# Performance work log

Measured on AMD Instinct MI355X. Metric: run time of the kernel, lower is better.

Reference implementation:

```python
import jax, jax.numpy as jnp
import numpy as np

EMBED = 768
HEADS = 12
FFN = 3072
EPS = 1e-5

def _linear_params(key, din, dout):
    k1, k2 = jax.random.split(key)
    s = 1.0 / np.sqrt(din)
    W = jax.random.uniform(k1, (din, dout), minval=-s, maxval=s, dtype=jnp.float32)
    b = jax.random.uniform(k2, (dout,), minval=-s, maxval=s, dtype=jnp.float32)
    return W, b

def setup_inputs() -> dict:
    key = jax.random.key(0)
    ks = jax.random.split(key, 8)
    x = jax.random.normal(ks[0], (1, 4096, EMBED), dtype=jnp.float32)
    Wq, bq = _linear_params(ks[1], EMBED, EMBED)
    Wk, bk = _linear_params(ks[2], EMBED, EMBED)
    Wv, bv = _linear_params(ks[3], EMBED, EMBED)
    Wo, bo = _linear_params(ks[4], EMBED, EMBED)
    W1, b1 = _linear_params(ks[5], EMBED, FFN)
    W2, b2 = _linear_params(ks[6], FFN, EMBED)
    ln1_g = jnp.ones((EMBED,), jnp.float32); ln1_b = jnp.zeros((EMBED,), jnp.float32)
    ln2_g = jnp.ones((EMBED,), jnp.float32); ln2_b = jnp.zeros((EMBED,), jnp.float32)
    return {"x": x, "Wq": Wq, "bq": bq, "Wk": Wk, "bk": bk, "Wv": Wv, "bv": bv,
            "Wo": Wo, "bo": bo, "ln1_g": ln1_g, "ln1_b": ln1_b,
            "ln2_g": ln2_g, "ln2_b": ln2_b, "W1": W1, "b1": b1, "W2": W2, "b2": b2}

def _layernorm(x, g, b):
    mu = jnp.mean(x, axis=-1, keepdims=True)
    var = jnp.mean(jnp.square(x - mu), axis=-1, keepdims=True)
    return (x - mu) * jax.lax.rsqrt(var + EPS) * g + b

def _block(x, Wq, bq, Wk, bk, Wv, bv, Wo, bo, ln1_g, ln1_b, ln2_g, ln2_b, W1, b1, W2, b2):
    B, T, C = x.shape
    H = HEADS
    D = C // H
    # pre-LN
    h = _layernorm(x, ln1_g, ln1_b)
    # naive causal self-attention with explicit [B,H,T,T] scores (as in source)
    q = (h @ Wq + bq).reshape(B, T, H, D).transpose(0, 2, 1, 3)  # bhtd
    k = (h @ Wk + bk).reshape(B, T, H, D).transpose(0, 2, 1, 3)
    v = (h @ Wv + bv).reshape(B, T, H, D).transpose(0, 2, 1, 3)
    scores = jnp.einsum('bhqd,bhkd->bhqk', q, k) / jnp.sqrt(jnp.float32(D))
    causal = jnp.tril(jnp.ones((T, T), dtype=bool))  # True = keep
    scores = jnp.where(causal, scores, -jnp.inf)
    attn = jax.nn.softmax(scores, axis=-1)
    ctx = jnp.einsum('bhqk,bhkd->bhqd', attn, v)
    ctx = ctx.transpose(0, 2, 1, 3).reshape(B, T, C)
    y = ctx @ Wo + bo
    x = y + h  # residual onto ln1 output (source adds to post-LN x)
    # second LN + MLP
    h2 = _layernorm(x, ln2_g, ln2_b)
    m = jax.nn.gelu(h2 @ W1 + b1, approximate=False) @ W2 + b2
    return m + h2

def reference(x, Wq, bq, Wk, bk, Wv, bv, Wo, bo, ln1_g, ln1_b, ln2_g, ln2_b, W1, b1, W2, b2):
    return _block(x, Wq, bq, Wk, bk, Wv, bv, Wo, bo, ln1_g, ln1_b, ln2_g, ln2_b, W1, b1, W2, b2)
```

## Files before the change

kernel.cpp:

```cpp
#include <hip/hip_runtime.h>
#include <math.h>

#define EMBED 768
#define FFN_D 3072
#define TSEQ 4096
#define NHEAD 12
#define DHEAD 64
#define CQKV 2304
#define NSPLIT 4
#define NQITEMS 192
#define SC2Q 0.180336880111120419f

typedef _Float16 f16;
typedef __attribute__((ext_vector_type(2))) _Float16 f16x2;
typedef __attribute__((ext_vector_type(4))) _Float16 f16x4;
typedef __attribute__((ext_vector_type(8))) _Float16 f16x8;
typedef __attribute__((ext_vector_type(4))) float f32x4;

#if __has_builtin(__builtin_amdgcn_exp2f)
#define EXP2(x) __builtin_amdgcn_exp2f(x)
#else
#define EXP2(x) exp2f(x)
#endif

__device__ __forceinline__ f16x2 pkrtz(float a, float b) {
    return __builtin_bit_cast(f16x2, __builtin_amdgcn_cvt_pkrtz(a, b));
}

__device__ __forceinline__ void gload16(const f16* g, f16* lds) {
    __builtin_amdgcn_global_load_lds((const __attribute__((address_space(1))) void*)g,
                                     (__attribute__((address_space(3))) void*)lds, 16, 0, 0);
}

__global__ __launch_bounds__(256) void prep_kernel(const float* __restrict__ Wq,
                                                   const float* __restrict__ Wk,
                                                   const float* __restrict__ Wv,
                                                   const float* __restrict__ Wo,
                                                   const float* __restrict__ W1,
                                                   const float* __restrict__ W2,
                                                   const float* __restrict__ bq,
                                                   const float* __restrict__ bk,
                                                   const float* __restrict__ bv,
                                                   f16* __restrict__ WqkvT,
                                                   f16* __restrict__ WoT,
                                                   f16* __restrict__ W1T,
                                                   f16* __restrict__ W2T,
                                                   float* __restrict__ bqkv) {
    const int b = blockIdx.x;
    const int t = threadIdx.x;
    if (b == 1728) {
#pragma unroll
        for (int i = 0; i < 9; i++) {
            int idx = i * 256 + t;
            if (idx < 768) bqkv[idx] = bq[idx];
            else if (idx < 1536) bqkv[idx] = bk[idx - 768];
            else if (idx < 2304) bqkv[idx] = bv[idx - 1536];
        }
        return;
    }
    const float* W; f16* WT; int din, dout, local;
    if (b < 144)       { W = Wq; WT = WqkvT;                 din = 768;  dout = 768;  local = b; }
    else if (b < 288)  { W = Wk; WT = WqkvT + 768 * 768;     din = 768;  dout = 768;  local = b - 144; }
    else if (b < 432)  { W = Wv; WT = WqkvT + 2 * 768 * 768; din = 768;  dout = 768;  local = b - 288; }
    else if (b < 576)  { W = Wo; WT = WoT;                   din = 768;  dout = 768;  local = b - 432; }
    else if (b < 1152) { W = W1; WT = W1T;                   din = 768;  dout = 3072; local = b - 576; }
    else               { W = W2; WT = W2T;                   din = 3072; dout = 768;  local = b - 1152; }
    const int ntx = dout / 64;
    const int j0 = (local % ntx) * 64;
    const int i0 = (local / ntx) * 64;
    __shared__ float tile[64][65];
    const int tx = t & 63;
    const int ty = t >> 6;
#pragma unroll
    for (int rr = ty; rr < 64; rr += 4)
        tile[rr][tx] = W[(size_t)(i0 + rr) * dout + j0 + tx];
    __syncthreads();
    const int half = t & 31;
    const int rw = t >> 5;
#pragma unroll
    for (int rr = rw; rr < 64; rr += 8) {
        f16x2 v = {(f16)tile[2 * half][rr], (f16)tile[2 * half + 1][rr]};
        *(f16x2*)&WT[(size_t)(j0 + rr) * din + i0 + 2 * half] = v;
    }
}

__global__ __launch_bounds__(256) void ln_kernel(const float* __restrict__ x,
                                                 const float* __restrict__ g,
                                                 const float* __restrict__ b,
                                                 f16* __restrict__ hh) {
    const int row = blockIdx.x;
    const float* xr = x + (size_t)row * EMBED;
    const int t = threadIdx.x;
    float v0 = xr[t], v1 = xr[t + 256], v2 = xr[t + 512];
    float s = v0 + v1 + v2;
#pragma unroll
    for (int m = 1; m < 64; m <<= 1) s += __shfl_xor(s, m);
    __shared__ float red[4], red2[4];
    const int wid = t >> 6, lane = t & 63;
    if (lane == 0) red[wid] = s;
    __syncthreads();
    float mean = (red[0] + red[1] + red[2] + red[3]) * (1.0f / 768.0f);
    float d0 = v0 - mean, d1 = v1 - mean, d2 = v2 - mean;
    float ss = d0 * d0 + d1 * d1 + d2 * d2;
#pragma unroll
    for (int m = 1; m < 64; m <<= 1) ss += __shfl_xor(ss, m);
    if (lane == 0) red2[wid] = ss;
    __syncthreads();
    float inv = rsqrtf((red2[0] + red2[1] + red2[2] + red2[3]) * (1.0f / 768.0f) + 1e-5f);
    size_t base = (size_t)row * EMBED;
    hh[base + t]       = (f16)(d0 * inv * g[t] + b[t]);
    hh[base + t + 256] = (f16)(d1 * inv * g[t + 256] + b[t + 256]);
    hh[base + t + 512] = (f16)(d2 * inv * g[t + 512] + b[t + 512]);
}

template <int EPI, int BM, int BN>
__global__ __launch_bounds__(256) void gemm_kernel(const f16* __restrict__ A,
                                                   const f16* __restrict__ BT,
                                                   const float* __restrict__ bias,
                                                   const f16* __restrict__ resh,
                                                   float* __restrict__ outf,
                                                   f16* __restrict__ outh,
                                                   f16* __restrict__ vtout,
                                                   int M, int N, int K) {
    constexpr int IM = BM / 32;
    constexpr int JN = BN / 32;
    __shared__ __align__(16) f16 As[BM][64];
    __shared__ __align__(16) f16 Bs[BN][64];
    const int t = threadIdx.x;
    const int m0 = blockIdx.y * BM;
    const int n0 = blockIdx.x * BN;
    const int wid = t >> 6;
    const int lane = t & 63;
    const int wm = (wid >> 1) * (BM / 2);
    const int wn = (wid & 1) * (BN / 2);
    const int lr = lane & 15;
    const int quad = lane >> 4;
    const int sr = lane >> 3;
    const int scn = (lane & 7) ^ sr;
    const int xv = lr & 7;

    f32x4 zero = {0.f, 0.f, 0.f, 0.f};
    f32x4 acc[IM][JN];
#pragma unroll
    for (int i = 0; i < IM; i++)
#pragma unroll
        for (int j = 0; j < JN; j++) acc[i][j] = zero;

    const f16* Ap = A + (size_t)(m0 + wid * (BM / 4) + sr) * K + scn * 8;
    const f16* Bp = BT + (size_t)(n0 + wid * (BN / 4) + sr) * K + scn * 8;

    for (int k0 = 0; k0 < K; k0 += 64) {
        __syncthreads();
#pragma unroll
        for (int c = 0; c < BM / 32; c++)
            gload16(Ap + (size_t)(c * 8) * K + k0, &As[wid * (BM / 4) + c * 8][0]);
#pragma unroll
        for (int c = 0; c < BN / 32; c++)
            gload16(Bp + (size_t)(c * 8) * K + k0, &Bs[wid * (BN / 4) + c * 8][0]);
        __syncthreads();
#pragma unroll
        for (int ks = 0; ks < 2; ks++) {
            f16x8 af[IM], bf[JN];
#pragma unroll
            for (int i = 0; i < IM; i++)
                af[i] = *(const f16x8*)&As[wm + i * 16 + lr][((ks * 4 + quad) ^ xv) * 8];
#pragma unroll
            for (int j = 0; j < JN; j++)
                bf[j] = *(const f16x8*)&Bs[wn + j * 16 + lr][((ks * 4 + quad) ^ xv) * 8];
#pragma unroll
            for (int i = 0; i < IM; i++)
#pragma unroll
                for (int j = 0; j < JN; j++)
                    acc[i][j] = __builtin_amdgcn_mfma_f32_16x16x32_f16(bf[j], af[i], acc[i][j], 0, 0, 0);
        }
    }

    const bool vsec = (EPI == 0) && (n0 >= 2 * EMBED);
#pragma unroll
    for (int i = 0; i < IM; i++) {
        const int row = m0 + wm + i * 16 + lr;
#pragma unroll
        for (int j = 0; j < JN; j++) {
            const int col = n0 + wn + j * 16 + quad * 4;
            const float4 bv = *(const float4*)&bias[col];
            float v0 = acc[i][j][0] + bv.x;
            float v1 = acc[i][j][1] + bv.y;
            float v2 = acc[i][j][2] + bv.z;
            float v3 = acc[i][j][3] + bv.w;
            const size_t idx = (size_t)row * N + col;
            if (EPI == 0) {
                if (vsec) {
                    const int c0 = col - 2 * EMBED;
                    vtout[(size_t)(c0 + 0) * TSEQ + row] = (f16)v0;
                    vtout[(size_t)(c0 + 1) * TSEQ + row] = (f16)v1;
                    vtout[(size_t)(c0 + 2) * TSEQ + row] = (f16)v2;
                    vtout[(size_t)(c0 + 3) * TSEQ + row] = (f16)v3;
                } else {
                    const float qs = (col < EMBED) ? SC2Q : 1.0f;
                    f16x4 hv = {(f16)(v0 * qs), (f16)(v1 * qs), (f16)(v2 * qs), (f16)(v3 * qs)};
                    *(f16x4*)&outh[idx] = hv;
                }
            } else if (EPI == 1) {
                const f16x4 rr = *(const f16x4*)&resh[idx];
                f32x4 ov = {v0 + (float)rr[0], v1 + (float)rr[1], v2 + (float)rr[2], v3 + (float)rr[3]};
                *(f32x4*)&outf[idx] = ov;
            } else {
                f16x4 hv = {(f16)(0.5f * v0 * (1.0f + erff(v0 * 0.70710678118654752f))),
                            (f16)(0.5f * v1 * (1.0f + erff(v1 * 0.70710678118654752f))),
                            (f16)(0.5f * v2 * (1.0f + erff(v2 * 0.70710678118654752f))),
                            (f16)(0.5f * v3 * (1.0f + erff(v3 * 0.70710678118654752f)))};
                *(f16x4*)&outh[idx] = hv;
            }
        }
    }
}

__global__ __launch_bounds__(256) void attn_kernel(const f16* __restrict__ qkv,
                                                   const f16* __restrict__ vT,
                                                   f16* __restrict__ OpartH,
                                                   float2* __restrict__ ml,
                                                   int* __restrict__ ctr) {
    __shared__ __align__(16) f16 Ks[2][64][72];
    __shared__ __align__(16) f16 Vt[2][64][72];
    __shared__ int s_item;
    const int t = threadIdx.x;
    const int wid = t >> 6;
    const int lane = t & 63;
    const int lr = lane & 15;
    const int quad = lane >> 4;
    const int srow = t >> 3;
    const int scol = (t & 7) * 8;
    const int pA = (t & 1) * 16 + ((t >> 1) & 1) * 4 + (t & 4) * 8;
    const int xq = blockIdx.x & 7;

    for (;;) {
        __syncthreads();
        if (t == 0) s_item = atomicAdd(&ctr[xq], 1);
        __syncthreads();
        const int item = s_item;
        if (item >= NQITEMS) return;
        const int qb = 31 - item / 6;
        const int u = xq * 6 + item % 6;
        const int h = u >> 2;
        const int sp = u & 3;
        const int q0 = qb * 128;

        const int nkb = 2 * qb + 2;
        const int chunk = (nkb + NSPLIT - 1) / NSPLIT;
        const int kb0 = sp * chunk;
        const int kb1 = min(nkb, kb0 + chunk);
        const int wrow0 = q0 + wid * 32;

        float m_i[2] = {-INFINITY, -INFINITY};
        float l_lane[2] = {0.f, 0.f};
        f32x4 zero = {0.f, 0.f, 0.f, 0.f};
        f32x4 o[4][2];
#pragma unroll
        for (int dt = 0; dt < 4; dt++)
#pragma unroll
            for (int qt = 0; qt < 2; qt++) o[dt][qt] = zero;

        f16x8 qf[2][2];
        int4 kreg[2], vreg[2];
        const f16* kbase = qkv + EMBED + (size_t)h * DHEAD;
        const f16* vbase = vT + (size_t)h * DHEAD * TSEQ;
        if (kb0 < kb1) {
#pragma unroll
            for (int qt = 0; qt < 2; qt++)
#pragma unroll
                for (int dh = 0; dh < 2; dh++)
                    qf[qt][dh] = *(const f16x8*)(qkv + (size_t)(wrow0 + qt * 16 + lr) * CQKV
                                                 + h * DHEAD + dh * 32 + quad * 8);
            const int k0 = kb0 * 64;
#pragma unroll
            for (int p = 0; p < 2; p++) {
                kreg[p] = *(const int4*)(kbase + (size_t)(k0 + p * 32 + srow) * CQKV + scol);
                vreg[p] = *(const int4*)(vbase + (size_t)(p * 32 + srow) * TSEQ + k0 + scol);
            }
#pragma unroll
            for (int p = 0; p < 2; p++) {
                *(int4*)&Ks[0][p * 32 + srow][scol] = kreg[p];
                *(int2*)&Vt[0][p * 32 + srow][pA]     = make_int2(vreg[p].x, vreg[p].y);
                *(int2*)&Vt[0][p * 32 + srow][pA + 8] = make_int2(vreg[p].z, vreg[p].w);
            }
            if (kb0 + 1 < kb1) {
                const int kn = k0 + 64;
#pragma unroll
                for (int p = 0; p < 2; p++) {
                    kreg[p] = *(const int4*)(kbase + (size_t)(kn + p * 32 + srow) * CQKV + scol);
                    vreg[p] = *(const int4*)(vbase + (size_t)(p * 32 + srow) * TSEQ + kn + scol);
                }
            }
        }
        __syncthreads();

        int bsel = 0;
        for (int kb = kb0; kb < kb1; ++kb, bsel ^= 1) {
            const int k0 = kb * 64;
            if (kb + 1 < kb1) {
#pragma unroll
                for (int p = 0; p < 2; p++) {
                    *(int4*)&Ks[bsel ^ 1][p * 32 + srow][scol] = kreg[p];
                    *(int2*)&Vt[bsel ^ 1][p * 32 + srow][pA]     = make_int2(vreg[p].x, vreg[p].y);
                    *(int2*)&Vt[bsel ^ 1][p * 32 + srow][pA + 8] = make_int2(vreg[p].z, vreg[p].w);
                }
                if (kb + 2 < kb1) {
                    const int kn = (kb + 2) * 64;
#pragma unroll
                    for (int p = 0; p < 2; p++) {
                        kreg[p] = *(const int4*)(kbase + (size_t)(kn + p * 32 + srow) * CQKV + scol);
                        vreg[p] = *(const int4*)(vbase + (size_t)(p * 32 + srow) * TSEQ + kn + scol);
                    }
                }
            }

            if (k0 <= wrow0 + 31) {
                f32x4 s[4][2];
#pragma unroll
                for (int kt = 0; kt < 4; kt++)
#pragma unroll
                    for (int qt = 0; qt < 2; qt++) s[kt][qt] = zero;
                __builtin_amdgcn_s_setprio(1);
#pragma unroll
                for (int dh = 0; dh < 2; dh++) {
#pragma unroll
                    for (int kt = 0; kt < 4; kt++) {
                        f16x8 kf = *(const f16x8*)&Ks[bsel][kt * 16 + lr][dh * 32 + quad * 8];
#pragma unroll
                        for (int qt = 0; qt < 2; qt++)
                            s[kt][qt] = __builtin_amdgcn_mfma_f32_16x16x32_f16(kf, qf[qt][dh], s[kt][qt], 0, 0, 0);
                    }
                }
                __builtin_amdgcn_s_setprio(0);
                if (k0 + 63 > wrow0) {
#pragma unroll
                    for (int kt = 0; kt < 4; kt++)
#pragma unroll
                        for (int qt = 0; qt < 2; qt++)
#pragma unroll
                            for (int r = 0; r < 4; r++) {
                                int key = k0 + kt * 16 + quad * 4 + r;
                                int row = wrow0 + qt * 16 + lr;
                                if (key > row) s[kt][qt][r] = -INFINITY;
                            }
                }
                float mx[2];
#pragma unroll
                for (int qt = 0; qt < 2; qt++) {
                    float m = -INFINITY;
#pragma unroll
                    for (int kt = 0; kt < 4; kt++)
#pragma unroll
                        for (int r = 0; r < 4; r++) m = fmaxf(m, s[kt][qt][r]);
                    m = fmaxf(m, __shfl_xor(m, 16));
                    m = fmaxf(m, __shfl_xor(m, 32));
                    mx[qt] = m;
                }
                if (__any((mx[0] > m_i[0] + 4.f) || (mx[1] > m_i[1] + 4.f))) {
#pragma unroll
                    for (int qt = 0; qt < 2; qt++) {
                        float mn = fmaxf(m_i[qt], mx[qt]);
                        float al = EXP2(m_i[qt] - mn);
                        m_i[qt] = mn;
                        l_lane[qt] *= al;
#pragma unroll
                        for (int dt = 0; dt < 4; dt++)
#pragma unroll
                            for (int r = 0; r < 4; r++) o[dt][qt][r] *= al;
                    }
                }
                union PW { f16x8 v8; f16x2 h2[4]; };
                PW pw[2][2];
                float rs[2] = {0.f, 0.f};
#pragma unroll
                for (int kt = 0; kt < 4; kt++)
#pragma unroll
                    for (int qt = 0; qt < 2; qt++) {
                        float p0 = EXP2(s[kt][qt][0] - m_i[qt]);
                        float p1 = EXP2(s[kt][qt][1] - m_i[qt]);
                        float p2 = EXP2(s[kt][qt][2] - m_i[qt]);
                        float p3 = EXP2(s[kt][qt][3] - m_i[qt]);
                        rs[qt] += (p0 + p1) + (p2 + p3);
                        pw[kt >> 1][qt].h2[(kt & 1) * 2]     = pkrtz(p0, p1);
                        pw[kt >> 1][qt].h2[(kt & 1) * 2 + 1] = pkrtz(p2, p3);
                    }
#pragma unroll
                for (int qt = 0; qt < 2; qt++) l_lane[qt] += rs[qt];
                __builtin_amdgcn_s_setprio(1);
#pragma unroll
                for (int s2 = 0; s2 < 2; s2++)
#pragma unroll
                    for (int dt = 0; dt < 4; dt++) {
                        f16x8 vf = *(const f16x8*)&Vt[bsel][dt * 16 + lr][s2 * 32 + quad * 8];
#pragma unroll
                        for (int qt = 0; qt < 2; qt++)
                            o[dt][qt] = __builtin_amdgcn_mfma_f32_16x16x32_f16(vf, pw[s2][qt].v8, o[dt][qt], 0, 0, 0);
                    }
                __builtin_amdgcn_s_setprio(0);
            }
            __syncthreads();
        }

        float l_i[2];
#pragma unroll
        for (int qt = 0; qt < 2; qt++) {
            float v2 = l_lane[qt];
            v2 += __shfl_xor(v2, 16);
            v2 += __shfl_xor(v2, 32);
            l_i[qt] = v2;
        }
        f16* ob = &Ks[0][0][0] + wid * (32 * 72);
#pragma unroll
        for (int qt = 0; qt < 2; qt++)
#pragma unroll
            for (int dt = 0; dt < 4; dt++) {
                f16x4 oh = {(f16)o[dt][qt][0], (f16)o[dt][qt][1], (f16)o[dt][qt][2], (f16)o[dt][qt][3]};
                *(f16x4*)&ob[(qt * 16 + lr) * 72 + dt * 16 + quad * 4] = oh;
            }
        const int rl = lane >> 3;
        const int ck = lane & 7;
#pragma unroll
        for (int i = 0; i < 4; i++) {
            const int row_l = rl + i * 8;
            f16x8 val = *(const f16x8*)&ob[row_l * 72 + ck * 8];
            *(f16x8*)&OpartH[((size_t)sp * TSEQ + wrow0 + row_l) * EMBED + h * DHEAD + ck * 8] = val;
        }
#pragma unroll
        for (int qt = 0; qt < 2; qt++)
            if (quad == 0) {
                int row = wrow0 + qt * 16 + lr;
                ml[((size_t)sp * TSEQ + row) * NHEAD + h] = make_float2(m_i[qt], l_i[qt]);
            }
    }
}

__global__ __launch_bounds__(128) void attn_merge_kernel(const f16* __restrict__ OpartH,
                                                         const float2* __restrict__ ml,
                                                         f16* __restrict__ ctx) {
    const int row = blockIdx.x;
    const int t = threadIdx.x;
    __shared__ float wgt[NSPLIT][NHEAD];
    if (t < NHEAD) {
        float m[NSPLIT], l[NSPLIT];
        float M = -INFINITY;
#pragma unroll
        for (int s = 0; s < NSPLIT; s++) {
            float2 v = ml[((size_t)s * TSEQ + row) * NHEAD + t];
            m[s] = v.x; l[s] = v.y;
            M = fmaxf(M, m[s]);
        }
        float L = 0.f;
        float w[NSPLIT];
#pragma unroll
        for (int s = 0; s < NSPLIT; s++) {
            w[s] = exp2f(m[s] - M);
            L += l[s] * w[s];
        }
        float rL = 1.0f / L;
#pragma unroll
        for (int s = 0; s < NSPLIT; s++) wgt[s][t] = w[s] * rL;
    }
    __syncthreads();
    if (t < 96) {
        const int h = t >> 3;
        float acc[8] = {0.f, 0.f, 0.f, 0.f, 0.f, 0.f, 0.f, 0.f};
#pragma unroll
        for (int s = 0; s < NSPLIT; s++) {
            const float w = wgt[s][h];
            f16x8 v = *(const f16x8*)&OpartH[((size_t)s * TSEQ + row) * EMBED + t * 8];
#pragma unroll
            for (int e = 0; e < 8; e++) acc[e] += w * (float)v[e];
        }
        f16x8 out;
#pragma unroll
        for (int e = 0; e < 8; e++) out[e] = (f16)acc[e];
        *(f16x8*)&ctx[(size_t)row * EMBED + t * 8] = out;
    }
}

extern "C" void kernel_launch(void* const* d_in, const int* in_sizes, int n_in,
                              void* d_out, int out_size, void* d_ws, size_t ws_size,
                              hipStream_t stream) {
    const float* x     = (const float*)d_in[0];
    const float* Wq    = (const float*)d_in[1];
    const float* bq    = (const float*)d_in[2];
    const float* Wk    = (const float*)d_in[3];
    const float* bk    = (const float*)d_in[4];
    const float* Wv    = (const float*)d_in[5];
    const float* bv    = (const float*)d_in[6];
    const float* Wo    = (const float*)d_in[7];
    const float* bo    = (const float*)d_in[8];
    const float* ln1_g = (const float*)d_in[9];
    const float* ln1_b = (const float*)d_in[10];
    const float* ln2_g = (const float*)d_in[11];
    const float* ln2_b = (const float*)d_in[12];
    const float* W1    = (const float*)d_in[13];
    const float* b1    = (const float*)d_in[14];
    const float* W2    = (const float*)d_in[15];
    const float* b2    = (const float*)d_in[16];

    char* p = (char*)d_ws;
    auto alloc = [&](size_t bytes) -> void* {
        void* r = (void*)p;
        p += (bytes + 255) & ~(size_t)255;
        return r;
    };
    f16*   WqkvT = (f16*)alloc((size_t)CQKV * EMBED * 2);
    f16*   WoT   = (f16*)alloc((size_t)EMBED * EMBED * 2);
    f16*   W1T   = (f16*)alloc((size_t)FFN_D * EMBED * 2);
    f16*   W2T   = (f16*)alloc((size_t)EMBED * FFN_D * 2);
    float* bqkv  = (float*)alloc((size_t)CQKV * 4);
    f16*   hh    = (f16*)alloc((size_t)TSEQ * EMBED * 2);
    f16*   qkv   = (f16*)alloc((size_t)TSEQ * CQKV * 2);
    f16*   vT    = (f16*)alloc((size_t)EMBED * TSEQ * 2);
    f16*   ctx   = (f16*)alloc((size_t)TSEQ * EMBED * 2);
    float* x2    = (float*)alloc((size_t)TSEQ * EMBED * 4);
    f16*   h2h   = (f16*)alloc((size_t)TSEQ * EMBED * 2);
    f16*   m1    = (f16*)alloc((size_t)TSEQ * FFN_D * 2);
    int*   ctr   = (int*)alloc(256);

    f16*    OpartH = m1;
    float2* mlbuf  = (float2*)x2;

    dim3 blk(256);
    prep_kernel<<<dim3(1729), blk, 0, stream>>>(Wq, Wk, Wv, Wo, W1, W2, bq, bk, bv,
                                                WqkvT, WoT, W1T, W2T, bqkv);
    ln_kernel<<<dim3(TSEQ), blk, 0, stream>>>(x, ln1_g, ln1_b, hh);
    gemm_kernel<0, 128, 128><<<dim3(CQKV / 128, TSEQ / 128), blk, 0, stream>>>(
        hh, WqkvT, bqkv, nullptr, nullptr, qkv, vT, TSEQ, CQKV, EMBED);
    (void)hipMemsetAsync(ctr, 0, 256, stream);
    attn_kernel<<<dim3(1024), blk, 0, stream>>>(qkv, vT, OpartH, mlbuf, ctr);
    attn_merge_kernel<<<dim3(TSEQ), dim3(128), 0, stream>>>(OpartH, mlbuf, ctx);
    gemm_kernel<1, 128, 128><<<dim3(EMBED / 128, TSEQ / 128), blk, 0, stream>>>(
        ctx, WoT, bo, hh, x2, nullptr, nullptr, TSEQ, EMBED, EMBED);
    ln_kernel<<<dim3(TSEQ), blk, 0, stream>>>(x2, ln2_g, ln2_b, h2h);
    gemm_kernel<2, 128, 128><<<dim3(FFN_D / 128, TSEQ / 128), blk, 0, stream>>>(
        h2h, W1T, b1, nullptr, nullptr, m1, nullptr, TSEQ, FFN_D, EMBED);
    gemm_kernel<1, 128, 128><<<dim3(EMBED / 128, TSEQ / 128), blk, 0, stream>>>(
        m1, W2T, b2, h2h, (float*)d_out, nullptr, nullptr, TSEQ, EMBED, FFN_D);
}
```

Baseline: 353.2 us.

## Split attention KV range eightfold, single-buffer LDS for occupancy, narrow output GEMM tiles

```diff
diff --git a/kernel.cpp b/kernel.cpp
--- a/kernel.cpp
+++ b/kernel.cpp
@@ -7,8 +7,8 @@
 #define NHEAD 12
 #define DHEAD 64
 #define CQKV 2304
-#define NSPLIT 4
-#define NQITEMS 192
+#define NSPLIT 8
+#define NQITEMS 384
 #define SC2Q 0.180336880111120419f
 
 typedef _Float16 f16;
@@ -215,13 +215,13 @@
     }
 }
 
-__global__ __launch_bounds__(256) void attn_kernel(const f16* __restrict__ qkv,
-                                                   const f16* __restrict__ vT,
-                                                   f16* __restrict__ OpartH,
-                                                   float2* __restrict__ ml,
-                                                   int* __restrict__ ctr) {
-    __shared__ __align__(16) f16 Ks[2][64][72];
-    __shared__ __align__(16) f16 Vt[2][64][72];
+__global__ __launch_bounds__(256, 6) void attn_kernel(const f16* __restrict__ qkv,
+                                                      const f16* __restrict__ vT,
+                                                      f16* __restrict__ OpartH,
+                                                      float2* __restrict__ ml,
+                                                      int* __restrict__ ctr) {
+    __shared__ __align__(16) f16 Ks[64][72];
+    __shared__ __align__(16) f16 Vt[64][72];
     __shared__ int s_item;
     const int t = threadIdx.x;
     const int wid = t >> 6;
@@ -239,10 +239,10 @@
         __syncthreads();
         const int item = s_item;
         if (item >= NQITEMS) return;
-        const int qb = 31 - item / 6;
-        const int u = xq * 6 + item % 6;
-        const int h = u >> 2;
-        const int sp = u & 3;
+        const int qb = 31 - item / 12;
+        const int u = xq * 12 + item % 12;
+        const int h = u >> 3;
+        const int sp = u & 7;
         const int q0 = qb * 128;
 
         const int nkb = 2 * qb + 2;
@@ -277,42 +277,26 @@
                 kreg[p] = *(const int4*)(kbase + (size_t)(k0 + p * 32 + srow) * CQKV + scol);
                 vreg[p] = *(const int4*)(vbase + (size_t)(p * 32 + srow) * TSEQ + k0 + scol);
             }
+        }
+
+        for (int kb = kb0; kb < kb1; ++kb) {
+            const int k0 = kb * 64;
+            __syncthreads();
 #pragma unroll
             for (int p = 0; p < 2; p++) {
-                *(int4*)&Ks[0][p * 32 + srow][scol] = kreg[p];
-                *(int2*)&Vt[0][p * 32 + srow][pA]     = make_int2(vreg[p].x, vreg[p].y);
-                *(int2*)&Vt[0][p * 32 + srow][pA + 8] = make_int2(vreg[p].z, vreg[p].w);
-            }
-            if (kb0 + 1 < kb1) {
-                const int kn = k0 + 64;
+                *(int4*)&Ks[p * 32 + srow][scol] = kreg[p];
+                *(int2*)&Vt[p * 32 + srow][pA]     = make_int2(vreg[p].x, vreg[p].y);
+                *(int2*)&Vt[p * 32 + srow][pA + 8] = make_int2(vreg[p].z, vreg[p].w);
+            }
+            __syncthreads();
+            if (kb + 1 < kb1) {
+                const int kn = (kb + 1) * 64;
 #pragma unroll
                 for (int p = 0; p < 2; p++) {
                     kreg[p] = *(const int4*)(kbase + (size_t)(kn + p * 32 + srow) * CQKV + scol);
                     vreg[p] = *(const int4*)(vbase + (size_t)(p * 32 + srow) * TSEQ + kn + scol);
                 }
             }
-        }
-        __syncthreads();
-
-        int bsel = 0;
-        for (int kb = kb0; kb < kb1; ++kb, bsel ^= 1) {
-            const int k0 = kb * 64;
-            if (kb + 1 < kb1) {
-#pragma unroll
-                for (int p = 0; p < 2; p++) {
-                    *(int4*)&Ks[bsel ^ 1][p * 32 + srow][scol] = kreg[p];
-                    *(int2*)&Vt[bsel ^ 1][p * 32 + srow][pA]     = make_int2(vreg[p].x, vreg[p].y);
-                    *(int2*)&Vt[bsel ^ 1][p * 32 + srow][pA + 8] = make_int2(vreg[p].z, vreg[p].w);
-                }
-                if (kb + 2 < kb1) {
-                    const int kn = (kb + 2) * 64;
-#pragma unroll
-                    for (int p = 0; p < 2; p++) {
-                        kreg[p] = *(const int4*)(kbase + (size_t)(kn + p * 32 + srow) * CQKV + scol);
-                        vreg[p] = *(const int4*)(vbase + (size_t)(p * 32 + srow) * TSEQ + kn + scol);
-                    }
-                }
-            }
 
             if (k0 <= wrow0 + 31) {
                 f32x4 s[4][2];
@@ -320,18 +304,16 @@
                 for (int kt = 0; kt < 4; kt++)
 #pragma unroll
                     for (int qt = 0; qt < 2; qt++) s[kt][qt] = zero;
-                __builtin_amdgcn_s_setprio(1);
 #pragma unroll
                 for (int dh = 0; dh < 2; dh++) {
 #pragma unroll
                     for (int kt = 0; kt < 4; kt++) {
-                        f16x8 kf = *(const f16x8*)&Ks[bsel][kt * 16 + lr][dh * 32 + quad * 8];
+                        f16x8 kf = *(const f16x8*)&Ks[kt * 16 + lr][dh * 32 + quad * 8];
 #pragma unroll
                         for (int qt = 0; qt < 2; qt++)
                             s[kt][qt] = __builtin_amdgcn_mfma_f32_16x16x32_f16(kf, qf[qt][dh], s[kt][qt], 0, 0, 0);
                     }
                 }
-                __builtin_amdgcn_s_setprio(0);
                 if (k0 + 63 > wrow0) {
 #pragma unroll
                     for (int kt = 0; kt < 4; kt++)
@@ -386,19 +368,16 @@
                     }
 #pragma unroll
                 for (int qt = 0; qt < 2; qt++) l_lane[qt] += rs[qt];
-                __builtin_amdgcn_s_setprio(1);
 #pragma unroll
                 for (int s2 = 0; s2 < 2; s2++)
 #pragma unroll
                     for (int dt = 0; dt < 4; dt++) {
-                        f16x8 vf = *(const f16x8*)&Vt[bsel][dt * 16 + lr][s2 * 32 + quad * 8];
+                        f16x8 vf = *(const f16x8*)&Vt[dt * 16 + lr][s2 * 32 + quad * 8];
 #pragma unroll
                         for (int qt = 0; qt < 2; qt++)
                             o[dt][qt] = __builtin_amdgcn_mfma_f32_16x16x32_f16(vf, pw[s2][qt].v8, o[dt][qt], 0, 0, 0);
                     }
-                __builtin_amdgcn_s_setprio(0);
-            }
-            __syncthreads();
+            }
         }
 
         float l_i[2];
@@ -409,7 +388,8 @@
             v2 += __shfl_xor(v2, 32);
             l_i[qt] = v2;
         }
-        f16* ob = &Ks[0][0][0] + wid * (32 * 72);
+        __syncthreads();
+        f16* ob = ((wid & 2) ? &Vt[0][0] : &Ks[0][0]) + (wid & 1) * (32 * 72);
 #pragma unroll
         for (int qt = 0; qt < 2; qt++)
 #pragma unroll
@@ -517,10 +497,10 @@
     float* x2    = (float*)alloc((size_t)TSEQ * EMBED * 4);
     f16*   h2h   = (f16*)alloc((size_t)TSEQ * EMBED * 2);
     f16*   m1    = (f16*)alloc((size_t)TSEQ * FFN_D * 2);
+    float2* mlbuf = (float2*)alloc((size_t)NSPLIT * TSEQ * NHEAD * sizeof(float2));
     int*   ctr   = (int*)alloc(256);
 
-    f16*    OpartH = m1;
-    float2* mlbuf  = (float2*)x2;
+    f16* OpartH = ctx;
 
     dim3 blk(256);
     prep_kernel<<<dim3(1729), blk, 0, stream>>>(Wq, Wk, Wv, Wo, W1, W2, bq, bk, bv,
@@ -529,13 +509,13 @@
     gemm_kernel<0, 128, 128><<<dim3(CQKV / 128, TSEQ / 128), blk, 0, stream>>>(
         hh, WqkvT, bqkv, nullptr, nullptr, qkv, vT, TSEQ, CQKV, EMBED);
     (void)hipMemsetAsync(ctr, 0, 256, stream);
-    attn_kernel<<<dim3(1024), blk, 0, stream>>>(qkv, vT, OpartH, mlbuf, ctr);
+    attn_kernel<<<dim3(1536), blk, 0, stream>>>(qkv, vT, OpartH, mlbuf, ctr);
     attn_merge_kernel<<<dim3(TSEQ), dim3(128), 0, stream>>>(OpartH, mlbuf, ctx);
-    gemm_kernel<1, 128, 128><<<dim3(EMBED / 128, TSEQ / 128), blk, 0, stream>>>(
+    gemm_kernel<1, 128, 64><<<dim3(EMBED / 64, TSEQ / 128), blk, 0, stream>>>(
         ctx, WoT, bo, hh, x2, nullptr, nullptr, TSEQ, EMBED, EMBED);
     ln_kernel<<<dim3(TSEQ), blk, 0, stream>>>(x2, ln2_g, ln2_b, h2h);
     gemm_kernel<2, 128, 128><<<dim3(FFN_D / 128, TSEQ / 128), blk, 0, stream>>>(
         h2h, W1T, b1, nullptr, nullptr, m1, nullptr, TSEQ, FFN_D, EMBED);
-    gemm_kernel<1, 128, 128><<<dim3(EMBED / 128, TSEQ / 128), blk, 0, stream>>>(
+    gemm_kernel<1, 128, 64><<<dim3(EMBED / 64, TSEQ / 128), blk, 0, stream>>>(
         m1, W2T, b2, h2h, (float*)d_out, nullptr, nullptr, TSEQ, EMBED, FFN_D);
 }
```

New measurement: 528.2 us. +49.5%, slower.
